# Performance work log

Measured on AMD Instinct MI355X. Metric: run time of the kernel, lower is better.

The kernel has to match this reference:

```python
import jax, jax.numpy as jnp
import numpy as np
from jax import lax

B, T, H, CTX, CONV_OUT = 32, 1536, 1024, 1024, 32


def setup_inputs() -> dict:
    key = jax.random.key(0)
    ks = jax.random.split(key, 10)
    s = 1.0 / np.sqrt(H)
    return {
        "decoder_output": jax.random.normal(ks[0], (B, 1, H), jnp.float32),
        "encoder_outputs": jax.random.normal(ks[1], (B, T, H), jnp.float32),
        "last_alignment": jax.random.uniform(ks[2], (B, T), jnp.float32),
        "W": jax.random.normal(ks[3], (CTX, H), jnp.float32) * s,
        "V": jax.random.normal(ks[4], (CTX, H), jnp.float32) * s,
        "U": jax.random.normal(ks[5], (CTX, CONV_OUT), jnp.float32) * (1.0 / np.sqrt(CONV_OUT)),
        "b": jax.random.uniform(ks[6], (CTX,), jnp.float32, -0.1, 0.1),
        "w": jax.random.normal(ks[7], (CTX,), jnp.float32) * (1.0 / np.sqrt(CTX)),
        "conv_w": jax.random.normal(ks[8], (CONV_OUT, 1, 3), jnp.float32) * 0.5,
        "conv_b": jax.random.normal(ks[9], (CONV_OUT,), jnp.float32) * 0.1,
    }


def reference(decoder_output, encoder_outputs, last_alignment, W, V, U, b, w, conv_w, conv_b):
    # location feature: Conv1d(1 -> conv_out, k=3, pad=1) over previous alignment
    conv = lax.conv_general_dilated(
        last_alignment[:, None, :], conv_w,
        window_strides=(1,), padding=[(1, 1)],
        dimension_numbers=("NCW", "OIW", "NCW"),
    ) + conv_b[None, :, None]                      # (B, conv_out, T)
    loc = jnp.transpose(conv, (0, 2, 1))           # (B, T, conv_out)

    # additive (Bahdanau) energies: (B,1,ctx) + (B,T,ctx) + (B,T,ctx) + (ctx,)
    e = jnp.tanh(
        jnp.einsum("bqh,ch->bqc", decoder_output, W)
        + jnp.einsum("bth,ch->btc", encoder_outputs, V)
        + jnp.einsum("btk,ck->btc", loc, U)
        + b
    )                                              # (B, T, ctx)
    scores = jnp.einsum("btc,c->bt", e, w)         # (B, T)
    alignment = jax.nn.softmax(scores, axis=-1)    # (B, T)
    context = jnp.einsum("bt,bth->bh", alignment, encoder_outputs)  # (B, H)
    return context, alignment
```

## Files before the change

kernel.cpp:

```cpp
#include <hip/hip_runtime.h>
#include <hip/hip_bf16.h>
#include <hip/hip_fp16.h>


constexpr int kB = 32, kT = 1536, kH = 1024, kC = 1024, kCO = 32;
constexpr int kM = kB * kT;
constexpr int kKb = 1088;

typedef _Float16 f16;
typedef _Float16 f16x8 __attribute__((ext_vector_type(8)));
typedef float f32x4 __attribute__((ext_vector_type(4)));

constexpr size_t WS_B     = 0;
constexpr size_t WS_LOC   = WS_B + (size_t)kC * kKb * 2;
constexpr size_t WS_ADD   = WS_LOC + (size_t)kM * 64 * 2;
constexpr size_t WS_SCORE = WS_ADD + (size_t)kB * kC * 4;
constexpr size_t WS_CTXP  = WS_SCORE + (size_t)4 * kM * 4;

__device__ __forceinline__ void gload16(const void* g, void* l) {
    __builtin_amdgcn_global_load_lds(
        (const __attribute__((address_space(1))) void*)g,
        (__attribute__((address_space(3))) void*)l, 16, 0, 0);
}

__global__ void k_prep_b2(const float* __restrict__ V, const float* __restrict__ U,
                          f16* __restrict__ Bf) {
    int c = blockIdx.x;
    for (int k = threadIdx.x; k < kKb; k += 256) {
        float v = (k < kH) ? V[(size_t)c * kH + k]
                : (k < kH + kCO) ? U[(size_t)c * kCO + (k - kH)] : 0.f;
        Bf[(size_t)c * kKb + k] = (f16)v;
    }
}

__global__ void k_loc(const float* __restrict__ la, const float* __restrict__ cw,
                      const float* __restrict__ cb, f16* __restrict__ locPad) {
    int m = blockIdx.x * 256 + threadIdx.x;
    int b = m / kT, t = m - b * kT;
    float x0 = (t > 0)      ? la[(size_t)b * kT + t - 1] : 0.f;
    float x1 = la[(size_t)b * kT + t];
    float x2 = (t < kT - 1) ? la[(size_t)b * kT + t + 1] : 0.f;
    union { f16 h[32]; int4 q[4]; } u;
#pragma unroll
    for (int k = 0; k < 32; ++k)
        u.h[k] = (f16)(cw[k * 3] * x0 + cw[k * 3 + 1] * x1 + cw[k * 3 + 2] * x2 + cb[k]);
    int4* dst = (int4*)(locPad + (size_t)m * 64);
    dst[0] = u.q[0]; dst[1] = u.q[1]; dst[2] = u.q[2]; dst[3] = u.q[3];
}

__global__ void k_prep_add(const float* __restrict__ dec, const float* __restrict__ W,
                           const float* __restrict__ bias, float* __restrict__ add) {
    __shared__ float dl[kH];
    int bb = blockIdx.x >> 2;
    int cc = (blockIdx.x & 3) * 256 + threadIdx.x;
    *(float4*)&dl[threadIdx.x * 4] = *(const float4*)&dec[(size_t)bb * kH + threadIdx.x * 4];
    __syncthreads();
    float acc = bias[cc];
    const float* wr = W + (size_t)cc * kH;
    for (int h = 0; h < kH; h += 4) {
        float4 wv = *(const float4*)&wr[h];
        acc += wv.x * dl[h] + wv.y * dl[h + 1] + wv.z * dl[h + 2] + wv.w * dl[h + 3];
    }
    add[(size_t)bb * kC + cc] = acc;
}

__launch_bounds__(512, 4)
__global__ void k_main(const float* __restrict__ enc, const f16* __restrict__ Bf,
                       const f16* __restrict__ locPad, const float* __restrict__ add,
                       const float* __restrict__ wvec, float* __restrict__ spart) {
    __shared__ __align__(16) char smem[69632];
    float* add_l = (float*)(smem + 65536);
    float* w_l   = (float*)(smem + 66560);
    float (*sred)[64][4] = (float (*)[64][4])(smem + 67584);

    const int tid = threadIdx.x, lane = tid & 63, wave = tid >> 6;
    const int wm = wave >> 2, wn = wave & 3;
    const int raw = blockIdx.x;
    const int lin = (raw & 7) * 192 + (raw >> 3);
    const int mt = lin >> 2, nt = lin & 3;
    const int m0 = mt * 128, n0 = nt * 256;
    const int bb = m0 / kT;

    if (tid < 256) {
        add_l[tid] = add[(size_t)bb * kC + n0 + tid];
        w_l[tid]   = wvec[n0 + tid];
    }

    f32x4 acc[4][4];
#pragma unroll
    for (int i = 0; i < 4; ++i)
#pragma unroll
        for (int j = 0; j < 4; ++j) acc[i][j] = (f32x4){0.f, 0.f, 0.f, 0.f};

    const int rA = lane >> 4;
    const float* aSrc[4];
#pragma unroll
    for (int j = 0; j < 4; ++j) {
        int gc = (lane & 15) ^ ((j * 4 + rA) & 15);
        aSrc[j] = enc + (size_t)(m0 + wave * 16 + j * 4 + rA) * kH + gc * 4;
    }
    const int rB = lane >> 3;
    const int gcB = (lane & 7) ^ (rB & 7);
    const f16* bSrc[4];
#pragma unroll
    for (int j = 0; j < 4; ++j)
        bSrc[j] = Bf + (size_t)(n0 + wave * 32 + j * 8 + rB) * kKb + gcB * 8;

    const unsigned aDst = wave * 4096u;
    const unsigned bDst = 32768u + wave * 4096u;
    const int g = lane >> 4, rl = lane & 15;

    for (int t = 0; t < 16; ++t) {
#pragma unroll
        for (int j = 0; j < 4; ++j) gload16(aSrc[j] + t * 64, smem + aDst + j * 1024);
#pragma unroll
        for (int j = 0; j < 4; ++j) gload16(bSrc[j] + t * 64, smem + bDst + j * 1024);
        __syncthreads();
#pragma unroll
        for (int kk = 0; kk < 2; ++kk) {
            f16x8 bfv[4];
#pragma unroll
            for (int ni = 0; ni < 4; ++ni)
                bfv[ni] = *(const f16x8*)(smem + 32768 + (wn * 64 + ni * 16 + rl) * 128
                                          + (((kk * 4 + g) ^ (rl & 7)) << 4));
#pragma unroll
            for (int mi = 0; mi < 4; ++mi) {
                const unsigned rowByte = (unsigned)((wm * 64 + mi * 16 + rl) * 256);
                float4 lo = *(const float4*)(smem + rowByte + (((kk * 8 + 2 * g) ^ rl) << 4));
                float4 hi = *(const float4*)(smem + rowByte + (((kk * 8 + 2 * g + 1) ^ rl) << 4));
                f16x8 ah;
                ah[0] = (f16)lo.x; ah[1] = (f16)lo.y; ah[2] = (f16)lo.z; ah[3] = (f16)lo.w;
                ah[4] = (f16)hi.x; ah[5] = (f16)hi.y; ah[6] = (f16)hi.z; ah[7] = (f16)hi.w;
#pragma unroll
                for (int ni = 0; ni < 4; ++ni)
                    acc[mi][ni] = __builtin_amdgcn_mfma_f32_16x16x32_f16(ah, bfv[ni], acc[mi][ni], 0, 0, 0);
            }
        }
        __syncthreads();
    }

    {
        const f16* tS0 = locPad + (size_t)(m0 + wave * 16 + 0 + rB) * 64 + gcB * 8;
        const f16* tS1 = locPad + (size_t)(m0 + wave * 16 + 8 + rB) * 64 + gcB * 8;
        gload16(tS0, smem + wave * 2048u);
        gload16(tS1, smem + wave * 2048u + 1024u);
#pragma unroll
        for (int j = 0; j < 4; ++j) gload16(bSrc[j] + 1024, smem + bDst + j * 1024);
        __syncthreads();
        f16x8 bfv[4];
#pragma unroll
        for (int ni = 0; ni < 4; ++ni)
            bfv[ni] = *(const f16x8*)(smem + 32768 + (wn * 64 + ni * 16 + rl) * 128
                                      + ((g ^ (rl & 7)) << 4));
#pragma unroll
        for (int mi = 0; mi < 4; ++mi) {
            f16x8 ah = *(const f16x8*)(smem + (wm * 64 + mi * 16 + rl) * 128
                                       + ((g ^ (rl & 7)) << 4));
#pragma unroll
            for (int ni = 0; ni < 4; ++ni)
                acc[mi][ni] = __builtin_amdgcn_mfma_f32_16x16x32_f16(ah, bfv[ni], acc[mi][ni], 0, 0, 0);
        }
        __syncthreads();
    }

#pragma unroll
    for (int mi = 0; mi < 4; ++mi) {
#pragma unroll
        for (int i = 0; i < 4; ++i) {
            float p = 0.f;
#pragma unroll
            for (int ni = 0; ni < 4; ++ni) {
                int cl = wn * 64 + ni * 16 + rl;
                float e = tanhf(acc[mi][ni][i] + add_l[cl]);
                p += e * w_l[cl];
            }
            p += __shfl_xor(p, 1);
            p += __shfl_xor(p, 2);
            p += __shfl_xor(p, 4);
            p += __shfl_xor(p, 8);
            if (rl == 0) sred[wm][mi * 16 + g * 4 + i][wn] = p;
        }
    }
    __syncthreads();
    if (tid < 128) {
        int r = tid & 63, w2 = tid >> 6;
        float s = sred[w2][r][0] + sred[w2][r][1] + sred[w2][r][2] + sred[w2][r][3];
        spart[(size_t)nt * kM + m0 + tid] = s;
    }
}

__global__ void k_softmax(const float* __restrict__ spart, float* __restrict__ out_align) {
    __shared__ float red[256];
    int b = blockIdx.x, tid = threadIdx.x;
    float v[6];
    float mx = -1e30f;
#pragma unroll
    for (int i = 0; i < 6; ++i) {
        size_t idx = (size_t)b * kT + tid + i * 256;
        float s = spart[idx] + spart[kM + idx] + spart[2 * (size_t)kM + idx] + spart[3 * (size_t)kM + idx];
        v[i] = s; mx = fmaxf(mx, s);
    }
    red[tid] = mx; __syncthreads();
    for (int o = 128; o > 0; o >>= 1) { if (tid < o) red[tid] = fmaxf(red[tid], red[tid + o]); __syncthreads(); }
    mx = red[0]; __syncthreads();
    float sum = 0.f;
#pragma unroll
    for (int i = 0; i < 6; ++i) { v[i] = expf(v[i] - mx); sum += v[i]; }
    red[tid] = sum; __syncthreads();
    for (int o = 128; o > 0; o >>= 1) { if (tid < o) red[tid] += red[tid + o]; __syncthreads(); }
    float inv = 1.f / red[0];
#pragma unroll
    for (int i = 0; i < 6; ++i)
        out_align[(size_t)b * kT + tid + i * 256] = v[i] * inv;
}

__global__ void k_ctx_part(const float* __restrict__ enc, const float* __restrict__ align,
                           float* __restrict__ cpart) {
    __shared__ float al[192];
    int ci = blockIdx.x, b = blockIdx.y, tid = threadIdx.x;
    if (tid < 192) al[tid] = align[(size_t)b * kT + ci * 192 + tid];
    __syncthreads();
    float4 acc = {0.f, 0.f, 0.f, 0.f};
    const float* ep = enc + ((size_t)b * kT + (size_t)ci * 192) * kH + tid * 4;
    for (int t = 0; t < 192; ++t) {
        float a = al[t];
        float4 e = *(const float4*)(ep + (size_t)t * kH);
        acc.x += a * e.x; acc.y += a * e.y; acc.z += a * e.z; acc.w += a * e.w;
    }
    *(float4*)&cpart[((size_t)ci * kB + b) * kH + tid * 4] = acc;
}

__global__ void k_ctx_red(const float* __restrict__ cpart, float* __restrict__ out_ctx) {
    int idx = blockIdx.x * 256 + threadIdx.x;
    float s = 0.f;
#pragma unroll
    for (int ci = 0; ci < 8; ++ci) s += cpart[(size_t)ci * kB * kH + idx];
    out_ctx[idx] = s;
}

extern "C" void kernel_launch(void* const* d_in, const int* in_sizes, int n_in,
                              void* d_out, int out_size, void* d_ws, size_t ws_size,
                              hipStream_t stream) {
    const float* dec  = (const float*)d_in[0];
    const float* enc  = (const float*)d_in[1];
    const float* la   = (const float*)d_in[2];
    const float* W    = (const float*)d_in[3];
    const float* V    = (const float*)d_in[4];
    const float* U    = (const float*)d_in[5];
    const float* bias = (const float*)d_in[6];
    const float* wv   = (const float*)d_in[7];
    const float* cw   = (const float*)d_in[8];
    const float* cb   = (const float*)d_in[9];

    char* ws = (char*)d_ws;
    f16* Bf      = (f16*)(ws + WS_B);
    f16* locPad  = (f16*)(ws + WS_LOC);
    float* add   = (float*)(ws + WS_ADD);
    float* spart = (float*)(ws + WS_SCORE);
    float* cpart = (float*)(ws + WS_CTXP);

    float* out_ctx   = (float*)d_out;
    float* out_align = (float*)d_out + kB * kH;

    hipLaunchKernelGGL(k_prep_b2,  dim3(kC),            dim3(256), 0, stream, V, U, Bf);
    hipLaunchKernelGGL(k_loc,      dim3(kM / 256),      dim3(256), 0, stream, la, cw, cb, locPad);
    hipLaunchKernelGGL(k_prep_add, dim3(kB * 4),        dim3(256), 0, stream, dec, W, bias, add);
    hipLaunchKernelGGL(k_main,     dim3((kM / 128) * 4), dim3(512), 0, stream, enc, Bf, locPad, add, wv, spart);
    hipLaunchKernelGGL(k_softmax,  dim3(kB),            dim3(256), 0, stream, spart, out_align);
    hipLaunchKernelGGL(k_ctx_part, dim3(8, kB),         dim3(256), 0, stream, enc, out_align, cpart);
    hipLaunchKernelGGL(k_ctx_red,  dim3(kB * kH / 256), dim3(256), 0, stream, cpart, out_ctx);
}
```

Baseline: 221.3 us.

## Shrink main GEMM tile to 128x128 with 4 waves and add MFMA priority hints

```diff
diff --git a/kernel.cpp b/kernel.cpp
--- a/kernel.cpp
+++ b/kernel.cpp
@@ -15,7 +15,7 @@
 constexpr size_t WS_LOC   = WS_B + (size_t)kC * kKb * 2;
 constexpr size_t WS_ADD   = WS_LOC + (size_t)kM * 64 * 2;
 constexpr size_t WS_SCORE = WS_ADD + (size_t)kB * kC * 4;
-constexpr size_t WS_CTXP  = WS_SCORE + (size_t)4 * kM * 4;
+constexpr size_t WS_CTXP  = WS_SCORE + (size_t)8 * kM * 4;
 
 __device__ __forceinline__ void gload16(const void* g, void* l) {
     __builtin_amdgcn_global_load_lds(
@@ -64,24 +64,24 @@
     add[(size_t)bb * kC + cc] = acc;
 }
 
-__launch_bounds__(512, 4)
+__launch_bounds__(256, 3)
 __global__ void k_main(const float* __restrict__ enc, const f16* __restrict__ Bf,
                        const f16* __restrict__ locPad, const float* __restrict__ add,
                        const float* __restrict__ wvec, float* __restrict__ spart) {
-    __shared__ __align__(16) char smem[69632];
-    float* add_l = (float*)(smem + 65536);
-    float* w_l   = (float*)(smem + 66560);
-    float (*sred)[64][4] = (float (*)[64][4])(smem + 67584);
+    __shared__ __align__(16) char smem[51200];
+    float* add_l = (float*)(smem + 49152);
+    float* w_l   = (float*)(smem + 49664);
+    float (*sred)[64][2] = (float (*)[64][2])(smem + 50176);
 
     const int tid = threadIdx.x, lane = tid & 63, wave = tid >> 6;
-    const int wm = wave >> 2, wn = wave & 3;
+    const int wm = wave >> 1, wn = wave & 1;
     const int raw = blockIdx.x;
-    const int lin = (raw & 7) * 192 + (raw >> 3);
-    const int mt = lin >> 2, nt = lin & 3;
-    const int m0 = mt * 128, n0 = nt * 256;
+    const int lin = (raw & 7) * 384 + (raw >> 3);
+    const int mt = lin >> 3, nt = lin & 7;
+    const int m0 = mt * 128, n0 = nt * 128;
     const int bb = m0 / kT;
 
-    if (tid < 256) {
+    if (tid < 128) {
         add_l[tid] = add[(size_t)bb * kC + n0 + tid];
         w_l[tid]   = wvec[n0 + tid];
     }
@@ -93,28 +93,31 @@
         for (int j = 0; j < 4; ++j) acc[i][j] = (f32x4){0.f, 0.f, 0.f, 0.f};
 
     const int rA = lane >> 4;
-    const float* aSrc[4];
+    const float* aS[8];
+#pragma unroll
+    for (int j = 0; j < 8; ++j) {
+        int row = wave * 32 + j * 4 + rA;
+        int gc = (lane & 15) ^ (row & 15);
+        aS[j] = enc + (size_t)(m0 + row) * kH + gc * 4;
+    }
+    const int rB = lane >> 3;
+    const f16* bS[4];
 #pragma unroll
     for (int j = 0; j < 4; ++j) {
-        int gc = (lane & 15) ^ ((j * 4 + rA) & 15);
-        aSrc[j] = enc + (size_t)(m0 + wave * 16 + j * 4 + rA) * kH + gc * 4;
-    }
-    const int rB = lane >> 3;
-    const int gcB = (lane & 7) ^ (rB & 7);
-    const f16* bSrc[4];
-#pragma unroll
-    for (int j = 0; j < 4; ++j)
-        bSrc[j] = Bf + (size_t)(n0 + wave * 32 + j * 8 + rB) * kKb + gcB * 8;
-
-    const unsigned aDst = wave * 4096u;
+        int row = wave * 32 + j * 8 + rB;
+        int gc = (lane & 7) ^ (row & 7);
+        bS[j] = Bf + (size_t)(n0 + row) * kKb + gc * 8;
+    }
+    const unsigned aDst = wave * 8192u;
     const unsigned bDst = 32768u + wave * 4096u;
+
     const int g = lane >> 4, rl = lane & 15;
 
     for (int t = 0; t < 16; ++t) {
 #pragma unroll
-        for (int j = 0; j < 4; ++j) gload16(aSrc[j] + t * 64, smem + aDst + j * 1024);
-#pragma unroll
-        for (int j = 0; j < 4; ++j) gload16(bSrc[j] + t * 64, smem + bDst + j * 1024);
+        for (int j = 0; j < 8; ++j) gload16(aS[j] + t * 64, smem + aDst + j * 1024);
+#pragma unroll
+        for (int j = 0; j < 4; ++j) gload16(bS[j] + t * 64, smem + bDst + j * 1024);
         __syncthreads();
 #pragma unroll
         for (int kk = 0; kk < 2; ++kk) {
@@ -125,33 +128,40 @@
                                           + (((kk * 4 + g) ^ (rl & 7)) << 4));
 #pragma unroll
             for (int mi = 0; mi < 4; ++mi) {
-                const unsigned rowByte = (unsigned)((wm * 64 + mi * 16 + rl) * 256);
-                float4 lo = *(const float4*)(smem + rowByte + (((kk * 8 + 2 * g) ^ rl) << 4));
-                float4 hi = *(const float4*)(smem + rowByte + (((kk * 8 + 2 * g + 1) ^ rl) << 4));
+                const unsigned rowB = (unsigned)((wm * 64 + mi * 16 + rl) * 256);
+                const int c = kk * 8 + g * 2;
+                float4 lo = *(const float4*)(smem + rowB + ((c ^ rl) << 4));
+                float4 hi = *(const float4*)(smem + rowB + (((c + 1) ^ rl) << 4));
                 f16x8 ah;
                 ah[0] = (f16)lo.x; ah[1] = (f16)lo.y; ah[2] = (f16)lo.z; ah[3] = (f16)lo.w;
                 ah[4] = (f16)hi.x; ah[5] = (f16)hi.y; ah[6] = (f16)hi.z; ah[7] = (f16)hi.w;
+                __builtin_amdgcn_s_setprio(1);
 #pragma unroll
                 for (int ni = 0; ni < 4; ++ni)
                     acc[mi][ni] = __builtin_amdgcn_mfma_f32_16x16x32_f16(ah, bfv[ni], acc[mi][ni], 0, 0, 0);
+                __builtin_amdgcn_s_setprio(0);
             }
         }
         __syncthreads();
     }
 
     {
-        const f16* tS0 = locPad + (size_t)(m0 + wave * 16 + 0 + rB) * 64 + gcB * 8;
-        const f16* tS1 = locPad + (size_t)(m0 + wave * 16 + 8 + rB) * 64 + gcB * 8;
-        gload16(tS0, smem + wave * 2048u);
-        gload16(tS1, smem + wave * 2048u + 1024u);
-#pragma unroll
-        for (int j = 0; j < 4; ++j) gload16(bSrc[j] + 1024, smem + bDst + j * 1024);
+#pragma unroll
+        for (int j = 0; j < 4; ++j) {
+            int row = wave * 32 + j * 8 + rB;
+            int gc = (lane & 7) ^ (row & 7);
+            const f16* tS = locPad + (size_t)(m0 + row) * 64 + gc * 8;
+            gload16(tS, smem + wave * 4096u + j * 1024);
+        }
+#pragma unroll
+        for (int j = 0; j < 4; ++j) gload16(bS[j] + 1024, smem + bDst + j * 1024);
         __syncthreads();
         f16x8 bfv[4];
 #pragma unroll
         for (int ni = 0; ni < 4; ++ni)
             bfv[ni] = *(const f16x8*)(smem + 32768 + (wn * 64 + ni * 16 + rl) * 128
                                       + ((g ^ (rl & 7)) << 4));
+        __builtin_amdgcn_s_setprio(1);
 #pragma unroll
         for (int mi = 0; mi < 4; ++mi) {
             f16x8 ah = *(const f16x8*)(smem + (wm * 64 + mi * 16 + rl) * 128
@@ -160,6 +170,7 @@
             for (int ni = 0; ni < 4; ++ni)
                 acc[mi][ni] = __builtin_amdgcn_mfma_f32_16x16x32_f16(ah, bfv[ni], acc[mi][ni], 0, 0, 0);
         }
+        __builtin_amdgcn_s_setprio(0);
         __syncthreads();
     }
 
@@ -184,7 +195,7 @@
     __syncthreads();
     if (tid < 128) {
         int r = tid & 63, w2 = tid >> 6;
-        float s = sred[w2][r][0] + sred[w2][r][1] + sred[w2][r][2] + sred[w2][r][3];
+        float s = sred[w2][r][0] + sred[w2][r][1];
         spart[(size_t)nt * kM + m0 + tid] = s;
     }
 }
@@ -197,7 +208,9 @@
 #pragma unroll
     for (int i = 0; i < 6; ++i) {
         size_t idx = (size_t)b * kT + tid + i * 256;
-        float s = spart[idx] + spart[kM + idx] + spart[2 * (size_t)kM + idx] + spart[3 * (size_t)kM + idx];
+        float s = 0.f;
+#pragma unroll
+        for (int p = 0; p < 8; ++p) s += spart[(size_t)p * kM + idx];
         v[i] = s; mx = fmaxf(mx, s);
     }
     red[tid] = mx; __syncthreads();
@@ -265,7 +278,7 @@
     hipLaunchKernelGGL(k_prep_b2,  dim3(kC),            dim3(256), 0, stream, V, U, Bf);
     hipLaunchKernelGGL(k_loc,      dim3(kM / 256),      dim3(256), 0, stream, la, cw, cb, locPad);
     hipLaunchKernelGGL(k_prep_add, dim3(kB * 4),        dim3(256), 0, stream, dec, W, bias, add);
-    hipLaunchKernelGGL(k_main,     dim3((kM / 128) * 4), dim3(512), 0, stream, enc, Bf, locPad, add, wv, spart);
+    hipLaunchKernelGGL(k_main,     dim3((kM / 128) * 8), dim3(256), 0, stream, enc, Bf, locPad, add, wv, spart);
     hipLaunchKernelGGL(k_softmax,  dim3(kB),            dim3(256), 0, stream, spart, out_align);
     hipLaunchKernelGGL(k_ctx_part, dim3(8, kB),         dim3(256), 0, stream, enc, out_align, cpart);
     hipLaunchKernelGGL(k_ctx_red,  dim3(kB * kH / 256), dim3(256), 0, stream, cpart, out_ctx);
```

Measured after the change: 239.0 us. 8.0% more time.
